# Kernel optimization log

Hardware: AMD Instinct MI355X
Metric: run time of the kernel (lower is better)

## Reference

```python
import jax, jax.numpy as jnp
import numpy as np

WIN = (2, 7, 7)
SHIFT = (1, 3, 3)
D, H, W = 8, 56, 56
C, NH = 128, 4
B = 8
N = WIN[0] * WIN[1] * WIN[2]  # 98


def _relative_position_index():
    d, h, w = np.meshgrid(np.arange(WIN[0]), np.arange(WIN[1]), np.arange(WIN[2]), indexing='ij')
    coords = np.stack([d.ravel(), h.ravel(), w.ravel()])  # (3, N)
    rel = coords[:, :, None] - coords[:, None, :]  # (3, N, N)
    rel = rel.transpose(1, 2, 0).astype(np.int64)
    rel[:, :, 0] += WIN[0] - 1
    rel[:, :, 1] += WIN[1] - 1
    rel[:, :, 2] += WIN[2] - 1
    rel[:, :, 0] *= (2 * WIN[1] - 1) * (2 * WIN[2] - 1)
    rel[:, :, 1] *= 2 * WIN[2] - 1
    return rel.sum(-1).astype(np.int32)  # (N, N)


def _shift_mask():
    img = np.zeros((1, D, H, W, 1), dtype=np.float32)
    cnt = 0
    for ds in (slice(0, -WIN[0]), slice(-WIN[0], -SHIFT[0]), slice(-SHIFT[0], None)):
        for hs in (slice(0, -WIN[1]), slice(-WIN[1], -SHIFT[1]), slice(-SHIFT[1], None)):
            for ws in (slice(0, -WIN[2]), slice(-WIN[2], -SHIFT[2]), slice(-SHIFT[2], None)):
                img[:, ds, hs, ws, :] = cnt
                cnt += 1
    m = img.reshape(1, D // WIN[0], WIN[0], H // WIN[1], WIN[1], W // WIN[2], WIN[2], 1)
    m = m.transpose(0, 1, 3, 5, 2, 4, 6, 7).reshape(-1, N)  # (nW, N)
    diff = m[:, None, :] - m[:, :, None]
    return np.where(diff != 0, np.float32(-100.0), np.float32(0.0))  # (nW, N, N)


def setup_inputs() -> dict:
    key = jax.random.key(0)
    ks = jax.random.split(key, 6)
    nW = (D // WIN[0]) * (H // WIN[1]) * (W // WIN[2])  # 256
    B_ = B * nW  # 2048
    table_size = (2 * WIN[0] - 1) * (2 * WIN[1] - 1) * (2 * WIN[2] - 1)  # 507
    return {
        'x': jax.random.normal(ks[0], (B_, N, C), dtype=jnp.float32),
        'qkv_w': jax.random.normal(ks[1], (3 * C, C), dtype=jnp.float32) * 0.02,
        'qkv_b': jax.random.normal(ks[2], (3 * C,), dtype=jnp.float32) * 0.02,
        'rpb_table': jax.random.normal(ks[3], (table_size, NH), dtype=jnp.float32) * 0.02,
        'proj_w': jax.random.normal(ks[4], (C, C), dtype=jnp.float32) * 0.02,
        'proj_b': jax.random.normal(ks[5], (C,), dtype=jnp.float32) * 0.02,
        'rel_index': jnp.asarray(_relative_position_index()),
        'mask': jnp.asarray(_shift_mask()),
    }


def reference(x, qkv_w, qkv_b, rpb_table, proj_w, proj_b, rel_index, mask):
    B_, n, c = x.shape
    hd = c // NH
    scale = hd ** -0.5
    # qkv projection -> (B_, n, 3, NH, hd)
    qkv = (x @ qkv_w.T + qkv_b).reshape(B_, n, 3, NH, hd)
    qkv = jnp.transpose(qkv, (2, 0, 3, 1, 4))  # (3, B_, NH, n, hd)
    q, k, v = qkv[0], qkv[1], qkv[2]
    attn = jnp.einsum('bhnd,bhmd->bhnm', q * scale, k)  # (B_, NH, n, n)
    # relative position bias gather
    bias = rpb_table[rel_index[:n, :n].reshape(-1)].reshape(n, n, NH)
    attn = attn + jnp.transpose(bias, (2, 0, 1))[None]
    # shift mask add
    nW = mask.shape[0]
    attn = attn.reshape(B_ // nW, nW, NH, n, n) + mask[None, :, None]
    attn = jax.nn.softmax(attn.reshape(B_, NH, n, n), axis=-1)
    out = jnp.einsum('bhnm,bhmd->bhnd', attn, v)
    out = jnp.transpose(out, (0, 2, 1, 3)).reshape(B_, n, c)
    return out @ proj_w.T + proj_b
```

## Files before the change

kernel.cpp:

```cpp
#include <hip/hip_runtime.h>
#include <math.h>
#include <stdint.h>


#define LOG2E   1.4426950408889634f
#define MASKNEG (-144.26950408889634f)

typedef __attribute__((ext_vector_type(8))) short bf16x8;
typedef __attribute__((ext_vector_type(4))) float f32x4;

__device__ __forceinline__ unsigned short cvt1(float f) {
    __bf16 h = (__bf16)f;
    return __builtin_bit_cast(unsigned short, h);
}
__device__ __forceinline__ unsigned cvt2(float lo, float hi) {
    return (unsigned)cvt1(lo) | ((unsigned)cvt1(hi) << 16);
}

__device__ __forceinline__ int tok_code(int t) {
    int pd = t / 49;
    int r  = t - pd * 49;
    int ph = r / 7;
    int pw = r - ph * 7;
    return (pd >= 1 ? 1 : 0) | (ph >= 4 ? 2 : 0) | (pw >= 4 ? 4 : 0);
}

__device__ __forceinline__ float mterm(unsigned pk, int sh, unsigned ci, unsigned cls) {
    return ((((pk >> sh) & 255u) ^ ci) & cls) ? MASKNEG : 0.f;
}

__device__ __forceinline__ int swz(int row, int col) {
    return row * 128 + (((col >> 3) ^ (row & 7)) << 3) + (col & 7);
}

template<bool BIG>
__global__ void prep_kernel(const float* __restrict__ qkv_w,
                            const float* __restrict__ proj_w,
                            const float* __restrict__ rpb_table,
                            const int*   __restrict__ rel_index,
                            unsigned short* __restrict__ wqkv,
                            unsigned short* __restrict__ wproj,
                            void* __restrict__ btab) {
    int tid = blockIdx.x * blockDim.x + threadIdx.x;
    int stride = gridDim.x * blockDim.x;
    for (int i = tid; i < 384 * 128; i += stride) wqkv[i]  = cvt1(qkv_w[i]);
    for (int i = tid; i < 128 * 128; i += stride) wproj[i] = cvt1(proj_w[i]);
    if constexpr (BIG) {
        float* bm = (float*)btab;
        for (int idx = tid; idx < 32 * 112 * 112; idx += stride) {
            int ch = idx / 12544; int r = idx - ch * 12544;
            int i  = r / 112;     int j = r - i * 112;
            int cls = ch >> 2, h = ch & 3;
            float v;
            if (i < 98) {
                if (j < 98) {
                    float bias = rpb_table[rel_index[i * 98 + j] * 4 + h];
                    bool  msk  = (((unsigned)tok_code(i) ^ (unsigned)tok_code(j)) & (unsigned)cls) != 0;
                    v = bias * LOG2E + (msk ? MASKNEG : 0.f);
                } else v = -INFINITY;
            } else v = 0.f;
            bm[idx] = v;
        }
    } else {
        unsigned short* biasL = (unsigned short*)btab;
        for (int idx = tid; idx < 4 * 112 * 112; idx += stride) {
            int h = idx / 12544; int r = idx - h * 12544;
            int i = r / 112;     int j = r - i * 112;
            float v;
            if (i < 98) v = (j < 98) ? rpb_table[rel_index[i * 98 + j] * 4 + h] * LOG2E
                                     : -INFINITY;
            else v = 0.f;
            biasL[idx] = cvt1(v);
        }
    }
}

template<bool BIG>
__global__ __launch_bounds__(1024)
void swin_main(const float* __restrict__ x,
               const float* __restrict__ qkv_b,
               const float* __restrict__ proj_b,
               const unsigned short* __restrict__ wqkv,
               const unsigned short* __restrict__ wproj,
               const void* __restrict__ btab,
               float* __restrict__ out)
{
    extern __shared__ unsigned short lds[];
    unsigned short* q_lds  = lds;
    unsigned short* k_lds  = lds + 14336;
    unsigned short* vT_lds = lds + 28672;
    unsigned short* xo_lds = lds + 45056;
    unsigned short* p_lds  = lds + 59392;

    const int b    = blockIdx.x;
    const int tid  = threadIdx.x;
    const int wv   = tid >> 6;
    const int lane = tid & 63;
    const int l4   = lane >> 4;
    const int lc   = lane & 15;

    {
        int idx2 = tid * 2;
        int row  = idx2 >> 4;
        int c    = 112 + (idx2 & 15);
        *(unsigned int*)(vT_lds + swz(row, c)) = 0u;
    }

    {
        const float* xb = x + (size_t)b * 12544;
        for (int idx = tid; idx < 3584; idx += 1024) {
            int tok = idx >> 5;
            int c   = (idx & 31) << 2;
            float4 v;
            if (tok < 98) v = *(const float4*)(xb + tok * 128 + c);
            else { v.x = 0.f; v.y = 0.f; v.z = 0.f; v.w = 0.f; }
            uint2 hv; hv.x = cvt2(v.x, v.y); hv.y = cvt2(v.z, v.w);
            *(uint2*)(xo_lds + swz(tok, c)) = hv;
        }
    }
    __syncthreads();

    {
        const int ct = wv;
        bf16x8 wf[4];
        f32x4  bias;
        const unsigned short* wrow = wqkv + (ct * 16 + lc) * 128;
#pragma unroll
        for (int kt = 0; kt < 4; ++kt) wf[kt] = *(const bf16x8*)(wrow + kt * 32 + l4 * 8);
#pragma unroll
        for (int r = 0; r < 4; ++r) bias[r] = qkv_b[ct * 16 + l4 * 4 + r];
        const bool  isq = (ct < 8);
        const float qs  = 0.17677669529663689f * LOG2E;
#pragma unroll
        for (int t = 0; t < 7; ++t) {
            bf16x8 xf[4];
#pragma unroll
            for (int kt = 0; kt < 4; ++kt)
                xf[kt] = *(bf16x8*)(xo_lds + swz(t * 16 + lc, kt * 32 + l4 * 8));
            f32x4 acc = bias;
#pragma unroll
            for (int kt = 0; kt < 4; ++kt)
                acc = __builtin_amdgcn_mfma_f32_16x16x32_bf16(wf[kt], xf[kt], acc, 0, 0, 0);
            int tok = t * 16 + lc;
            if (isq) {
                uint2 hv; hv.x = cvt2(acc[0] * qs, acc[1] * qs); hv.y = cvt2(acc[2] * qs, acc[3] * qs);
                *(uint2*)(q_lds + swz(tok, ct * 16 + l4 * 4)) = hv;
            } else {
                uint2 hv; hv.x = cvt2(acc[0], acc[1]); hv.y = cvt2(acc[2], acc[3]);
                *(uint2*)(k_lds + swz(tok, (ct - 8) * 16 + l4 * 4)) = hv;
            }
        }
        const int vd = (wv >> 1) * 16;
        bf16x8 wf2[4];
        const unsigned short* wrow2 = wqkv + (256 + vd + lc) * 128;
#pragma unroll
        for (int kt = 0; kt < 4; ++kt) wf2[kt] = *(const bf16x8*)(wrow2 + kt * 32 + l4 * 8);
        f32x4 bias2;
#pragma unroll
        for (int r = 0; r < 4; ++r) bias2[r] = qkv_b[256 + vd + l4 * 4 + r];
        const int t0 = (wv & 1) ? 4 : 0, t1 = (wv & 1) ? 7 : 4;
        for (int t = t0; t < t1; ++t) {
            bf16x8 xf[4];
#pragma unroll
            for (int kt = 0; kt < 4; ++kt)
                xf[kt] = *(bf16x8*)(xo_lds + swz(t * 16 + lc, kt * 32 + l4 * 8));
            f32x4 acc = bias2;
#pragma unroll
            for (int kt = 0; kt < 4; ++kt)
                acc = __builtin_amdgcn_mfma_f32_16x16x32_bf16(wf2[kt], xf[kt], acc, 0, 0, 0);
            int tok = t * 16 + lc;
            unsigned d0 = cvt2(acc[0], acc[1]);
            unsigned d1 = cvt2(acc[2], acc[3]);
            int rb = vd + l4 * 4;
            vT_lds[swz(rb + 0, tok)] = (unsigned short)d0;
            vT_lds[swz(rb + 1, tok)] = (unsigned short)(d0 >> 16);
            vT_lds[swz(rb + 2, tok)] = (unsigned short)d1;
            vT_lds[swz(rb + 3, tok)] = (unsigned short)(d1 >> 16);
        }
    }
    __syncthreads();

    const int wi  = b & 255;
    const unsigned int cls =
        ((wi >> 6) == 3 ? 1u : 0u) | (((wi >> 3) & 7) == 7 ? 2u : 0u) | ((wi & 7) == 7 ? 4u : 0u);

    unsigned int jcp[7];
    if constexpr (!BIG) {
#pragma unroll
        for (int jt = 0; jt < 7; ++jt) {
            int jb = jt * 16 + l4 * 4;
            unsigned int p = 0;
#pragma unroll
            for (int r = 0; r < 4; ++r) p |= (unsigned)tok_code(jb + r < 98 ? jb + r : 0) << (8 * r);
            jcp[jt] = p;
        }
    }

    unsigned short* myP = p_lds + wv * 1280;

    for (int pass = 0; pass < 2; ++pass) {
        int task = wv + (pass << 4);
        if (task >= 28) break;
        int h  = task / 7;
        int it = task - h * 7;
        const int i_tok = it * 16 + lc;
        const bf16x8 qfrag = *(bf16x8*)(q_lds + swz(i_tok, h * 32 + l4 * 8));

        f32x4 cvec[7];
        if constexpr (BIG) {
            const float* bmrow = (const float*)btab + ((size_t)((int)cls * 4 + h) * 112 + i_tok) * 112;
#pragma unroll
            for (int jt = 0; jt < 7; ++jt)
                cvec[jt] = *(const f32x4*)(bmrow + jt * 16 + l4 * 4);
        } else {
            const unsigned short* brow = (const unsigned short*)btab + (h * 112 + i_tok) * 112;
            const unsigned int ci = (unsigned)tok_code(i_tok < 98 ? i_tok : 0);
            ushort4 bb[7];
#pragma unroll
            for (int jt = 0; jt < 7; ++jt)
                bb[jt] = *(const ushort4*)(brow + jt * 16 + l4 * 4);
#pragma unroll
            for (int jt = 0; jt < 7; ++jt) {
                cvec[jt][0] = __builtin_bit_cast(float, (unsigned)bb[jt].x << 16) + mterm(jcp[jt], 0,  ci, cls);
                cvec[jt][1] = __builtin_bit_cast(float, (unsigned)bb[jt].y << 16) + mterm(jcp[jt], 8,  ci, cls);
                cvec[jt][2] = __builtin_bit_cast(float, (unsigned)bb[jt].z << 16) + mterm(jcp[jt], 16, ci, cls);
                cvec[jt][3] = __builtin_bit_cast(float, (unsigned)bb[jt].w << 16) + mterm(jcp[jt], 24, ci, cls);
            }
        }

        f32x4 s[7];
#pragma unroll
        for (int jt = 0; jt < 7; ++jt) {
            bf16x8 kfrag = *(bf16x8*)(k_lds + swz(jt * 16 + lc, h * 32 + l4 * 8));
            s[jt] = __builtin_amdgcn_mfma_f32_16x16x32_bf16(kfrag, qfrag, cvec[jt], 0, 0, 0);
        }

        float m = -INFINITY;
#pragma unroll
        for (int jt = 0; jt < 7; ++jt)
            m = fmaxf(m, fmaxf(fmaxf(s[jt][0], s[jt][1]), fmaxf(s[jt][2], s[jt][3])));
        m = fmaxf(m, __shfl_xor(m, 16));
        m = fmaxf(m, __shfl_xor(m, 32));

        float lsum = 0.f;
        f32x4 o0 = {0.f, 0.f, 0.f, 0.f}, o1 = {0.f, 0.f, 0.f, 0.f};
#pragma unroll
        for (int jt4 = 0; jt4 < 4; ++jt4) {
            unsigned short* pb = myP + (jt4 & 1) * 640;
#pragma unroll
            for (int sub = 0; sub < 2; ++sub) {
                int jt = jt4 * 2 + sub;
                uint2 pv;
                if (jt < 7) {
                    float p0 = exp2f(s[jt][0] - m);
                    float p1 = exp2f(s[jt][1] - m);
                    float p2 = exp2f(s[jt][2] - m);
                    float p3 = exp2f(s[jt][3] - m);
                    lsum += (p0 + p1) + (p2 + p3);
                    pv.x = cvt2(p0, p1); pv.y = cvt2(p2, p3);
                } else {
                    pv.x = 0u; pv.y = 0u;
                }
                *(uint2*)(pb + lc * 40 + sub * 16 + l4 * 4) = pv;
            }
            bf16x8 pfrag = *(bf16x8*)(pb + lc * 40 + l4 * 8);
            bf16x8 va = *(bf16x8*)(vT_lds + swz(h * 32 + lc,      jt4 * 32 + l4 * 8));
            bf16x8 vb = *(bf16x8*)(vT_lds + swz(h * 32 + 16 + lc, jt4 * 32 + l4 * 8));
            o0 = __builtin_amdgcn_mfma_f32_16x16x32_bf16(va, pfrag, o0, 0, 0, 0);
            o1 = __builtin_amdgcn_mfma_f32_16x16x32_bf16(vb, pfrag, o1, 0, 0, 0);
        }
        lsum += __shfl_xor(lsum, 16);
        lsum += __shfl_xor(lsum, 32);

        float inv = 1.0f / lsum;
        uint2 h0, h1;
        h0.x = cvt2(o0[0] * inv, o0[1] * inv); h0.y = cvt2(o0[2] * inv, o0[3] * inv);
        h1.x = cvt2(o1[0] * inv, o1[1] * inv); h1.y = cvt2(o1[2] * inv, o1[3] * inv);
        *(uint2*)(xo_lds + swz(i_tok, h * 32 + l4 * 4)) = h0;
        *(uint2*)(xo_lds + swz(i_tok, h * 32 + 16 + l4 * 4)) = h1;
    }
    __syncthreads();

    {
        const int ct = wv >> 1;
        bf16x8 pw[4];
#pragma unroll
        for (int kt = 0; kt < 4; ++kt)
            pw[kt] = *(const bf16x8*)(wproj + (ct * 16 + lc) * 128 + kt * 32 + l4 * 8);
        f32x4 pbias;
#pragma unroll
        for (int r = 0; r < 4; ++r) pbias[r] = proj_b[ct * 16 + l4 * 4 + r];

        float* ob = out + (size_t)b * 12544;
        const int t0 = (wv & 1) ? 4 : 0, t1 = (wv & 1) ? 7 : 4;
        for (int t = t0; t < t1; ++t) {
            f32x4 acc = pbias;
#pragma unroll
            for (int kt = 0; kt < 4; ++kt) {
                bf16x8 of = *(bf16x8*)(xo_lds + swz(t * 16 + lc, kt * 32 + l4 * 8));
                acc = __builtin_amdgcn_mfma_f32_16x16x32_bf16(pw[kt], of, acc, 0, 0, 0);
            }
            int tok = t * 16 + lc;
            if (tok < 98) {
                float4 st; st.x = acc[0]; st.y = acc[1]; st.z = acc[2]; st.w = acc[3];
                *(float4*)(ob + tok * 128 + ct * 16 + l4 * 4) = st;
            }
        }
    }
}

extern "C" void kernel_launch(void* const* d_in, const int* in_sizes, int n_in,
                              void* d_out, int out_size, void* d_ws, size_t ws_size,
                              hipStream_t stream) {
    const float* x       = (const float*)d_in[0];
    const float* qkv_w   = (const float*)d_in[1];
    const float* qkv_b   = (const float*)d_in[2];
    const float* rpb_tab = (const float*)d_in[3];
    const float* proj_w  = (const float*)d_in[4];
    const float* proj_b  = (const float*)d_in[5];
    const int*   rel_idx = (const int*)d_in[6];

    unsigned short* wqkv  = (unsigned short*)d_ws;
    unsigned short* wproj = (unsigned short*)((char*)d_ws + 98304);
    void*           btab  = (void*)((char*)d_ws + 131072);
    float*          out   = (float*)d_out;

    const bool big = ws_size >= (size_t)(131072 + 32 * 112 * 112 * 4);
    const int LDS_BYTES = 159744;

    if (big) {
        hipLaunchKernelGGL((prep_kernel<true>), dim3(512), dim3(256), 0, stream,
                           qkv_w, proj_w, rpb_tab, rel_idx, wqkv, wproj, btab);
        (void)hipFuncSetAttribute((const void*)(swin_main<true>),
                                  hipFuncAttributeMaxDynamicSharedMemorySize, LDS_BYTES);
        hipLaunchKernelGGL((swin_main<true>), dim3(2048), dim3(1024), LDS_BYTES, stream,
                           x, qkv_b, proj_b, wqkv, wproj, btab, out);
    } else {
        hipLaunchKernelGGL((prep_kernel<false>), dim3(512), dim3(256), 0, stream,
                           qkv_w, proj_w, rpb_tab, rel_idx, wqkv, wproj, btab);
        (void)hipFuncSetAttribute((const void*)(swin_main<false>),
                                  hipFuncAttributeMaxDynamicSharedMemorySize, LDS_BYTES);
        hipLaunchKernelGGL((swin_main<false>), dim3(2048), dim3(1024), LDS_BYTES, stream,
                           x, qkv_b, proj_b, wqkv, wproj, btab, out);
    }
}
```

Baseline: 137.3 us.

## Interleave attention tasks per wave, fuse V projection, new V-transpose swizzle

Each wave now issues the bias loads, QK^T MFMAs, softmax and PV for both of its attention tasks together instead of one after another, so more independent MFMA and memory work is in flight at once. The QK MFMAs run at raised wave priority via s_setprio. The V projection is folded into the Q/K projection loop so the x fragments from LDS are reused. The transposed V buffer gets a new swizzle (vswz) meant to cut LDS bank conflicts on the scalar transpose stores. In exchange, register pressure rises (two sets of score accumulators live at once), which may lower occupancy.

After: 160.2 us. +16.6%, slower.

```diff
diff --git a/kernel.cpp b/kernel.cpp
--- a/kernel.cpp
+++ b/kernel.cpp
@@ -31,6 +31,9 @@
 
 __device__ __forceinline__ int swz(int row, int col) {
     return row * 128 + (((col >> 3) ^ (row & 7)) << 3) + (col & 7);
+}
+__device__ __forceinline__ int vswz(int row, int col) {
+    return row * 128 + ((((col >> 3) ^ (row >> 2)) & 15) << 3) + (col & 7);
 }
 
 template<bool BIG>
@@ -99,11 +102,11 @@
     const int l4   = lane >> 4;
     const int lc   = lane & 15;
 
-    {
-        int idx2 = tid * 2;
-        int row  = idx2 >> 4;
-        int c    = 112 + (idx2 & 15);
-        *(unsigned int*)(vT_lds + swz(row, c)) = 0u;
+    if (tid < 512) {
+        int row = tid >> 2;
+        int c   = 112 + (tid & 3) * 4;
+        uint2 z; z.x = 0u; z.y = 0u;
+        *(uint2*)(vT_lds + vswz(row, c)) = z;
     }
 
     {
@@ -122,26 +125,35 @@
 
     {
         const int ct = wv;
-        bf16x8 wf[4];
-        f32x4  bias;
-        const unsigned short* wrow = wqkv + (ct * 16 + lc) * 128;
-#pragma unroll
-        for (int kt = 0; kt < 4; ++kt) wf[kt] = *(const bf16x8*)(wrow + kt * 32 + l4 * 8);
-#pragma unroll
-        for (int r = 0; r < 4; ++r) bias[r] = qkv_b[ct * 16 + l4 * 4 + r];
+        const int vd = (wv >> 1) * 16;
+        bf16x8 wf[4], wf2[4];
+        f32x4  bias, bias2;
+        const unsigned short* wrow  = wqkv + (ct * 16 + lc) * 128;
+        const unsigned short* wrow2 = wqkv + (256 + vd + lc) * 128;
+#pragma unroll
+        for (int kt = 0; kt < 4; ++kt) {
+            wf[kt]  = *(const bf16x8*)(wrow  + kt * 32 + l4 * 8);
+            wf2[kt] = *(const bf16x8*)(wrow2 + kt * 32 + l4 * 8);
+        }
+#pragma unroll
+        for (int r = 0; r < 4; ++r) {
+            bias[r]  = qkv_b[ct * 16 + l4 * 4 + r];
+            bias2[r] = qkv_b[256 + vd + l4 * 4 + r];
+        }
         const bool  isq = (ct < 8);
         const float qs  = 0.17677669529663689f * LOG2E;
+        const int t0 = (wv & 1) ? 4 : 0, t1 = (wv & 1) ? 7 : 4;
 #pragma unroll
         for (int t = 0; t < 7; ++t) {
             bf16x8 xf[4];
 #pragma unroll
             for (int kt = 0; kt < 4; ++kt)
                 xf[kt] = *(bf16x8*)(xo_lds + swz(t * 16 + lc, kt * 32 + l4 * 8));
+            const int tok = t * 16 + lc;
             f32x4 acc = bias;
 #pragma unroll
             for (int kt = 0; kt < 4; ++kt)
                 acc = __builtin_amdgcn_mfma_f32_16x16x32_bf16(wf[kt], xf[kt], acc, 0, 0, 0);
-            int tok = t * 16 + lc;
             if (isq) {
                 uint2 hv; hv.x = cvt2(acc[0] * qs, acc[1] * qs); hv.y = cvt2(acc[2] * qs, acc[3] * qs);
                 *(uint2*)(q_lds + swz(tok, ct * 16 + l4 * 4)) = hv;
@@ -149,33 +161,16 @@
                 uint2 hv; hv.x = cvt2(acc[0], acc[1]); hv.y = cvt2(acc[2], acc[3]);
                 *(uint2*)(k_lds + swz(tok, (ct - 8) * 16 + l4 * 4)) = hv;
             }
-        }
-        const int vd = (wv >> 1) * 16;
-        bf16x8 wf2[4];
-        const unsigned short* wrow2 = wqkv + (256 + vd + lc) * 128;
-#pragma unroll
-        for (int kt = 0; kt < 4; ++kt) wf2[kt] = *(const bf16x8*)(wrow2 + kt * 32 + l4 * 8);
-        f32x4 bias2;
-#pragma unroll
-        for (int r = 0; r < 4; ++r) bias2[r] = qkv_b[256 + vd + l4 * 4 + r];
-        const int t0 = (wv & 1) ? 4 : 0, t1 = (wv & 1) ? 7 : 4;
-        for (int t = t0; t < t1; ++t) {
-            bf16x8 xf[4];
-#pragma unroll
-            for (int kt = 0; kt < 4; ++kt)
-                xf[kt] = *(bf16x8*)(xo_lds + swz(t * 16 + lc, kt * 32 + l4 * 8));
-            f32x4 acc = bias2;
-#pragma unroll
-            for (int kt = 0; kt < 4; ++kt)
-                acc = __builtin_amdgcn_mfma_f32_16x16x32_bf16(wf2[kt], xf[kt], acc, 0, 0, 0);
-            int tok = t * 16 + lc;
-            unsigned d0 = cvt2(acc[0], acc[1]);
-            unsigned d1 = cvt2(acc[2], acc[3]);
-            int rb = vd + l4 * 4;
-            vT_lds[swz(rb + 0, tok)] = (unsigned short)d0;
-            vT_lds[swz(rb + 1, tok)] = (unsigned short)(d0 >> 16);
-            vT_lds[swz(rb + 2, tok)] = (unsigned short)d1;
-            vT_lds[swz(rb + 3, tok)] = (unsigned short)(d1 >> 16);
+            if (t >= t0 && t < t1) {
+                f32x4 acc2 = bias2;
+#pragma unroll
+                for (int kt = 0; kt < 4; ++kt)
+                    acc2 = __builtin_amdgcn_mfma_f32_16x16x32_bf16(wf2[kt], xf[kt], acc2, 0, 0, 0);
+                const int rb = vd + l4 * 4;
+#pragma unroll
+                for (int r = 0; r < 4; ++r)
+                    vT_lds[vswz(rb + r, tok)] = cvt1(acc2[r]);
+            }
         }
     }
     __syncthreads();
@@ -197,87 +192,109 @@
     }
 
     unsigned short* myP = p_lds + wv * 1280;
-
-    for (int pass = 0; pass < 2; ++pass) {
-        int task = wv + (pass << 4);
-        if (task >= 28) break;
-        int h  = task / 7;
-        int it = task - h * 7;
-        const int i_tok = it * 16 + lc;
-        const bf16x8 qfrag = *(bf16x8*)(q_lds + swz(i_tok, h * 32 + l4 * 8));
-
-        f32x4 cvec[7];
-        if constexpr (BIG) {
-            const float* bmrow = (const float*)btab + ((size_t)((int)cls * 4 + h) * 112 + i_tok) * 112;
+    const int nT = (wv < 12) ? 2 : 1;
+
+    {
+        f32x4  s[2][7];
+        bf16x8 qf[2];
+        int    hh[2], ii[2];
+
+#pragma unroll
+        for (int u = 0; u < 2; ++u) {
+            if (u >= nT) continue;
+            const int task = wv + (u << 4);
+            hh[u] = task / 7;
+            ii[u] = (task - hh[u] * 7) * 16 + lc;
+            qf[u] = *(bf16x8*)(q_lds + swz(ii[u], hh[u] * 32 + l4 * 8));
+            if constexpr (BIG) {
+                const float* bmrow = (const float*)btab
+                    + ((size_t)((int)cls * 4 + hh[u]) * 112 + ii[u]) * 112;
+#pragma unroll
+                for (int jt = 0; jt < 7; ++jt)
+                    s[u][jt] = *(const f32x4*)(bmrow + jt * 16 + l4 * 4);
+            } else {
+                const unsigned short* brow = (const unsigned short*)btab + (hh[u] * 112 + ii[u]) * 112;
+                const unsigned int ci = (unsigned)tok_code(ii[u] < 98 ? ii[u] : 0);
+#pragma unroll
+                for (int jt = 0; jt < 7; ++jt) {
+                    ushort4 bb = *(const ushort4*)(brow + jt * 16 + l4 * 4);
+                    s[u][jt][0] = __builtin_bit_cast(float, (unsigned)bb.x << 16) + mterm(jcp[jt], 0,  ci, cls);
+                    s[u][jt][1] = __builtin_bit_cast(float, (unsigned)bb.y << 16) + mterm(jcp[jt], 8,  ci, cls);
+                    s[u][jt][2] = __builtin_bit_cast(float, (unsigned)bb.z << 16) + mterm(jcp[jt], 16, ci, cls);
+                    s[u][jt][3] = __builtin_bit_cast(float, (unsigned)bb.w << 16) + mterm(jcp[jt], 24, ci, cls);
+                }
+            }
+        }
+
+        __builtin_amdgcn_s_setprio(1);
+#pragma unroll
+        for (int u = 0; u < 2; ++u) {
+            if (u >= nT) continue;
+#pragma unroll
+            for (int jt = 0; jt < 7; ++jt) {
+                bf16x8 kfrag = *(bf16x8*)(k_lds + swz(jt * 16 + lc, hh[u] * 32 + l4 * 8));
+                s[u][jt] = __builtin_amdgcn_mfma_f32_16x16x32_bf16(kfrag, qf[u], s[u][jt], 0, 0, 0);
+            }
+        }
+        __builtin_amdgcn_s_setprio(0);
+
+        float mx[2];
+#pragma unroll
+        for (int u = 0; u < 2; ++u) {
+            if (u >= nT) continue;
+            float m = -INFINITY;
 #pragma unroll
             for (int jt = 0; jt < 7; ++jt)
-                cvec[jt] = *(const f32x4*)(bmrow + jt * 16 + l4 * 4);
-        } else {
-            const unsigned short* brow = (const unsigned short*)btab + (h * 112 + i_tok) * 112;
-            const unsigned int ci = (unsigned)tok_code(i_tok < 98 ? i_tok : 0);
-            ushort4 bb[7];
-#pragma unroll
-            for (int jt = 0; jt < 7; ++jt)
-                bb[jt] = *(const ushort4*)(brow + jt * 16 + l4 * 4);
+                m = fmaxf(m, fmaxf(fmaxf(s[u][jt][0], s[u][jt][1]), fmaxf(s[u][jt][2], s[u][jt][3])));
+            m = fmaxf(m, __shfl_xor(m, 16));
+            m = fmaxf(m, __shfl_xor(m, 32));
+            mx[u] = m;
+        }
+
+        uint2 pp[2][8];
+        float ls[2];
+#pragma unroll
+        for (int u = 0; u < 2; ++u) {
+            if (u >= nT) continue;
+            float l = 0.f;
 #pragma unroll
             for (int jt = 0; jt < 7; ++jt) {
-                cvec[jt][0] = __builtin_bit_cast(float, (unsigned)bb[jt].x << 16) + mterm(jcp[jt], 0,  ci, cls);
-                cvec[jt][1] = __builtin_bit_cast(float, (unsigned)bb[jt].y << 16) + mterm(jcp[jt], 8,  ci, cls);
-                cvec[jt][2] = __builtin_bit_cast(float, (unsigned)bb[jt].z << 16) + mterm(jcp[jt], 16, ci, cls);
-                cvec[jt][3] = __builtin_bit_cast(float, (unsigned)bb[jt].w << 16) + mterm(jcp[jt], 24, ci, cls);
-            }
-        }
-
-        f32x4 s[7];
-#pragma unroll
-        for (int jt = 0; jt < 7; ++jt) {
-            bf16x8 kfrag = *(bf16x8*)(k_lds + swz(jt * 16 + lc, h * 32 + l4 * 8));
-            s[jt] = __builtin_amdgcn_mfma_f32_16x16x32_bf16(kfrag, qfrag, cvec[jt], 0, 0, 0);
-        }
-
-        float m = -INFINITY;
-#pragma unroll
-        for (int jt = 0; jt < 7; ++jt)
-            m = fmaxf(m, fmaxf(fmaxf(s[jt][0], s[jt][1]), fmaxf(s[jt][2], s[jt][3])));
-        m = fmaxf(m, __shfl_xor(m, 16));
-        m = fmaxf(m, __shfl_xor(m, 32));
-
-        float lsum = 0.f;
-        f32x4 o0 = {0.f, 0.f, 0.f, 0.f}, o1 = {0.f, 0.f, 0.f, 0.f};
-#pragma unroll
-        for (int jt4 = 0; jt4 < 4; ++jt4) {
-            unsigned short* pb = myP + (jt4 & 1) * 640;
-#pragma unroll
-            for (int sub = 0; sub < 2; ++sub) {
-                int jt = jt4 * 2 + sub;
-                uint2 pv;
-                if (jt < 7) {
-                    float p0 = exp2f(s[jt][0] - m);
-                    float p1 = exp2f(s[jt][1] - m);
-                    float p2 = exp2f(s[jt][2] - m);
-                    float p3 = exp2f(s[jt][3] - m);
-                    lsum += (p0 + p1) + (p2 + p3);
-                    pv.x = cvt2(p0, p1); pv.y = cvt2(p2, p3);
-                } else {
-                    pv.x = 0u; pv.y = 0u;
-                }
-                *(uint2*)(pb + lc * 40 + sub * 16 + l4 * 4) = pv;
-            }
-            bf16x8 pfrag = *(bf16x8*)(pb + lc * 40 + l4 * 8);
-            bf16x8 va = *(bf16x8*)(vT_lds + swz(h * 32 + lc,      jt4 * 32 + l4 * 8));
-            bf16x8 vb = *(bf16x8*)(vT_lds + swz(h * 32 + 16 + lc, jt4 * 32 + l4 * 8));
-            o0 = __builtin_amdgcn_mfma_f32_16x16x32_bf16(va, pfrag, o0, 0, 0, 0);
-            o1 = __builtin_amdgcn_mfma_f32_16x16x32_bf16(vb, pfrag, o1, 0, 0, 0);
-        }
-        lsum += __shfl_xor(lsum, 16);
-        lsum += __shfl_xor(lsum, 32);
-
-        float inv = 1.0f / lsum;
-        uint2 h0, h1;
-        h0.x = cvt2(o0[0] * inv, o0[1] * inv); h0.y = cvt2(o0[2] * inv, o0[3] * inv);
-        h1.x = cvt2(o1[0] * inv, o1[1] * inv); h1.y = cvt2(o1[2] * inv, o1[3] * inv);
-        *(uint2*)(xo_lds + swz(i_tok, h * 32 + l4 * 4)) = h0;
-        *(uint2*)(xo_lds + swz(i_tok, h * 32 + 16 + l4 * 4)) = h1;
+                float p0 = exp2f(s[u][jt][0] - mx[u]);
+                float p1 = exp2f(s[u][jt][1] - mx[u]);
+                float p2 = exp2f(s[u][jt][2] - mx[u]);
+                float p3 = exp2f(s[u][jt][3] - mx[u]);
+                l += (p0 + p1) + (p2 + p3);
+                pp[u][jt].x = cvt2(p0, p1);
+                pp[u][jt].y = cvt2(p2, p3);
+            }
+            pp[u][7].x = 0u; pp[u][7].y = 0u;
+            l += __shfl_xor(l, 16);
+            l += __shfl_xor(l, 32);
+            ls[u] = l;
+        }
+
+#pragma unroll
+        for (int u = 0; u < 2; ++u) {
+            if (u >= nT) continue;
+            f32x4 o0 = {0.f,0.f,0.f,0.f}, o1 = {0.f,0.f,0.f,0.f};
+#pragma unroll
+            for (int jt4 = 0; jt4 < 4; ++jt4) {
+                unsigned short* pb = myP + (jt4 & 1) * 640;
+                *(uint2*)(pb + lc * 40 + l4 * 4)      = pp[u][jt4 * 2];
+                *(uint2*)(pb + lc * 40 + 16 + l4 * 4) = pp[u][jt4 * 2 + 1];
+                bf16x8 pfrag = *(bf16x8*)(pb + lc * 40 + l4 * 8);
+                bf16x8 va = *(bf16x8*)(vT_lds + vswz(hh[u] * 32 + lc,      jt4 * 32 + l4 * 8));
+                bf16x8 vb = *(bf16x8*)(vT_lds + vswz(hh[u] * 32 + 16 + lc, jt4 * 32 + l4 * 8));
+                o0 = __builtin_amdgcn_mfma_f32_16x16x32_bf16(va, pfrag, o0, 0, 0, 0);
+                o1 = __builtin_amdgcn_mfma_f32_16x16x32_bf16(vb, pfrag, o1, 0, 0, 0);
+            }
+            const float inv = 1.0f / ls[u];
+            uint2 h0, h1;
+            h0.x = cvt2(o0[0] * inv, o0[1] * inv); h0.y = cvt2(o0[2] * inv, o0[3] * inv);
+            h1.x = cvt2(o1[0] * inv, o1[1] * inv); h1.y = cvt2(o1[2] * inv, o1[3] * inv);
+            *(uint2*)(xo_lds + swz(ii[u], hh[u] * 32 + l4 * 4)) = h0;
+            *(uint2*)(xo_lds + swz(ii[u], hh[u] * 32 + 16 + l4 * 4)) = h1;
+        }
     }
     __syncthreads();
 
```
